# Kernel optimization log

Measured on AMD Instinct MI355X. Metric: run time of the kernel, lower is better.

Reference implementation:

```python
import jax, jax.numpy as jnp
import numpy as np

BITS = 4            # bits per quantized weight
NPACK = 8           # 32-bit container / 4-bit values
CBITS = 32          # compression dtype bit width (int32)
GROUP = 128         # quantization group size along in_features
IN = 4096
OUT = 11008
BATCH = 32


def _dequant(packed_weight, scale):
    # Unpack signed int4 values: (p << (32 - 4*(e+1))) >> 28, arithmetic shift
    # sign-extends, matching the torch recover() path for weight_dtype=int8.
    e = jnp.arange(NPACK, dtype=jnp.int32)                      # [8]
    shifted = (packed_weight[:, :, None] << (CBITS - BITS * (e + 1))) >> (CBITS - BITS)  # [O, I/8, 8]
    w_int = shifted.reshape(OUT, IN).astype(jnp.int8)           # signed int4 in int8
    # Per-group scale: reshape to [O*I/GROUP, GROUP] * [O*I/GROUP, 1]
    w = w_int.astype(jnp.float32).reshape(-1, GROUP) * scale.reshape(-1, 1)
    return w.reshape(OUT, IN)


def setup_inputs() -> dict:
    key = jax.random.key(0)
    k1, k2, k3, k4 = jax.random.split(key, 4)
    x = jax.random.normal(k1, (BATCH, IN), dtype=jnp.float32)
    packed_weight = jax.random.randint(
        k2, (OUT, IN // NPACK), jnp.iinfo(jnp.int32).min, jnp.iinfo(jnp.int32).max,
        dtype=jnp.int32)
    scale = jax.random.uniform(k3, (OUT, IN // GROUP), dtype=jnp.float32,
                               minval=0.001, maxval=0.02)
    bias = jax.random.normal(k4, (OUT,), dtype=jnp.float32)
    return {"x": x, "packed_weight": packed_weight, "scale": scale, "bias": bias}


def reference(x, packed_weight, scale, bias):
    W = _dequant(packed_weight, scale)      # [OUT, IN] fp32
    return x @ W.T + bias                    # F.linear(x, W, bias)
```

## Files before the change

kernel.cpp:

```cpp
#include <hip/hip_runtime.h>

#define IN_F   4096
#define OUT_F  11008
#define BATCH  32
#define NG     32
#define PACKS  512
#define SLICES 4
#define SLICE_F (BATCH * OUT_F)

typedef __bf16 bf16x8_t __attribute__((ext_vector_type(8)));
typedef float  floatx4_t __attribute__((ext_vector_type(4)));

__global__ __launch_bounds__(256) void prep_x(const float* __restrict__ x,
                                              unsigned short* __restrict__ xp) {
  int c  = blockIdx.x * 256 + threadIdx.x;
  int mm = c & 31;
  int k0 = ((c >> 5) & 3) * 32 + ((c >> 7) & 3) * 8 + (c >> 9) * 128;
  const float* src = x + mm * IN_F + k0;
  float4 f0 = *(const float4*)(src);
  float4 f1 = *(const float4*)(src + 4);
  float v[8] = {f0.x, f0.y, f0.z, f0.w, f1.x, f1.y, f1.z, f1.w};
  union { unsigned short s[8]; uint4 u; } r;
#pragma unroll
  for (int j = 0; j < 8; ++j) {
    unsigned int u = __float_as_uint(v[j]);
    unsigned int rnd = ((u >> 16) & 1u) + 0x7fffu;
    r.s[j] = (unsigned short)((u + rnd) >> 16);
  }
  *(uint4*)(xp + c * 8) = r.u;
}

__device__ inline bf16x8_t unpack8(int p) {
  union { unsigned short u[8]; bf16x8_t v; } r;
#pragma unroll
  for (int j = 0; j < 8; ++j) {
    int nib = (p << (28 - 4 * j)) >> 28;
    float f = (float)nib;
    r.u[j] = (unsigned short)(__float_as_uint(f) >> 16);
  }
  return r.v;
}

__device__ inline bf16x8_t load_frag(const unsigned short* p) {
  union { uint4 u; bf16x8_t v; } x;
  x.u = *(const uint4*)p;
  return x.v;
}

__global__ __launch_bounds__(512) void wql_part(
    const int* __restrict__ pw, const float* __restrict__ scale,
    const unsigned short* __restrict__ xp, float* __restrict__ part) {
  __shared__ float lds[8][BATCH * 32];

  const int tid = threadIdx.x;
  const int l   = tid & 63;
  const int w   = tid >> 6;
  const int col = l & 15;
  const int q   = l >> 4;
  const int n0  = blockIdx.x * 32;
  const int kc  = blockIdx.y;
  const int nA  = n0 + col;
  const int nB  = n0 + 16 + col;
  const int gg  = kc * 8 + w;

  int4 pA = *(const int4*)(pw + nA * PACKS + gg * 16 + q * 4);
  int4 pB = *(const int4*)(pw + nB * PACKS + gg * 16 + q * 4);
  float sA = scale[nA * NG + gg];
  float sB = scale[nB * NG + gg];

  const unsigned short* ab = xp + (gg * 512 + q * 32 + col) * 8;
  bf16x8_t a0[4], a1[4];
#pragma unroll
  for (int t = 0; t < 4; ++t) {
    a0[t] = load_frag(ab + t * 1024);
    a1[t] = load_frag(ab + t * 1024 + 128);
  }

  floatx4_t t00 = {0.f, 0.f, 0.f, 0.f};
  floatx4_t t01 = {0.f, 0.f, 0.f, 0.f};
  floatx4_t t10 = {0.f, 0.f, 0.f, 0.f};
  floatx4_t t11 = {0.f, 0.f, 0.f, 0.f};
  int pAv[4] = {pA.x, pA.y, pA.z, pA.w};
  int pBv[4] = {pB.x, pB.y, pB.z, pB.w};
#pragma unroll
  for (int t = 0; t < 4; ++t) {
    bf16x8_t b0 = unpack8(pAv[t]);
    bf16x8_t b1 = unpack8(pBv[t]);
    t00 = __builtin_amdgcn_mfma_f32_16x16x32_bf16(a0[t], b0, t00, 0, 0, 0);
    t10 = __builtin_amdgcn_mfma_f32_16x16x32_bf16(a1[t], b0, t10, 0, 0, 0);
    t01 = __builtin_amdgcn_mfma_f32_16x16x32_bf16(a0[t], b1, t01, 0, 0, 0);
    t11 = __builtin_amdgcn_mfma_f32_16x16x32_bf16(a1[t], b1, t11, 0, 0, 0);
  }

#pragma unroll
  for (int r = 0; r < 4; ++r) {
    int row = q * 4 + r;
    lds[w][row * 32 + col]             = t00[r] * sA;
    lds[w][row * 32 + 16 + col]        = t01[r] * sB;
    lds[w][(16 + row) * 32 + col]      = t10[r] * sA;
    lds[w][(16 + row) * 32 + 16 + col] = t11[r] * sB;
  }
  __syncthreads();

  float* wsp = part + kc * SLICE_F + n0;
  for (int e = tid; e < BATCH * 32; e += 512) {
    int row = e >> 5, cl = e & 31;
    float s = lds[0][e] + lds[1][e] + lds[2][e] + lds[3][e]
            + lds[4][e] + lds[5][e] + lds[6][e] + lds[7][e];
    wsp[row * OUT_F + cl] = s;
  }
}

__global__ __launch_bounds__(256) void reduce_out(
    const float* __restrict__ part, const float* __restrict__ bias,
    float* __restrict__ out) {
  int e4 = blockIdx.x * 256 + threadIdx.x;
  int e  = e4 << 2;
  int o  = e % OUT_F;
  float4 s = *(const float4*)(bias + o);
#pragma unroll
  for (int k = 0; k < SLICES; ++k) {
    float4 p = *(const float4*)(part + k * SLICE_F + e);
    s.x += p.x; s.y += p.y; s.z += p.z; s.w += p.w;
  }
  *(float4*)(out + e) = s;
}

extern "C" void kernel_launch(void* const* d_in, const int* in_sizes, int n_in,
                              void* d_out, int out_size, void* d_ws, size_t ws_size,
                              hipStream_t stream) {
  const float* x     = (const float*)d_in[0];
  const int*   pw    = (const int*)d_in[1];
  const float* scale = (const float*)d_in[2];
  const float* bias  = (const float*)d_in[3];
  float* out = (float*)d_out;
  unsigned short* xp = (unsigned short*)d_ws;
  float* part = (float*)((char*)d_ws + (1 << 20));

  hipLaunchKernelGGL(prep_x, dim3(16384 / 256), dim3(256), 0, stream, x, xp);
  hipLaunchKernelGGL(wql_part, dim3(OUT_F / 32, 4), dim3(512), 0, stream,
                     pw, scale, xp, part);
  hipLaunchKernelGGL(reduce_out, dim3(BATCH * OUT_F / 4 / 256), dim3(256), 0,
                     stream, part, bias, out);
}
```

Measured before the change: 85.11 us.

## Fuse x bf16 conversion into main kernel via swizzled LDS staging

Removes the separate prep_x launch. Each block now loads its 32x1024 slice of fp32 x, converts it to bf16 and writes it into a 64KB LDS buffer with an XOR swizzle to avoid bank conflicts. MFMA A fragments are then read from LDS, and the same buffer is reused for the partial-sum reduction. This saves one kernel launch and a global round trip, but every block now redoes the x conversion (344 column blocks per k-slice), and the 64KB of LDS per block lowers occupancy.

```diff
diff --git a/kernel.cpp b/kernel.cpp
--- a/kernel.cpp
+++ b/kernel.cpp
@@ -11,25 +11,6 @@
 typedef __bf16 bf16x8_t __attribute__((ext_vector_type(8)));
 typedef float  floatx4_t __attribute__((ext_vector_type(4)));
 
-__global__ __launch_bounds__(256) void prep_x(const float* __restrict__ x,
-                                              unsigned short* __restrict__ xp) {
-  int c  = blockIdx.x * 256 + threadIdx.x;
-  int mm = c & 31;
-  int k0 = ((c >> 5) & 3) * 32 + ((c >> 7) & 3) * 8 + (c >> 9) * 128;
-  const float* src = x + mm * IN_F + k0;
-  float4 f0 = *(const float4*)(src);
-  float4 f1 = *(const float4*)(src + 4);
-  float v[8] = {f0.x, f0.y, f0.z, f0.w, f1.x, f1.y, f1.z, f1.w};
-  union { unsigned short s[8]; uint4 u; } r;
-#pragma unroll
-  for (int j = 0; j < 8; ++j) {
-    unsigned int u = __float_as_uint(v[j]);
-    unsigned int rnd = ((u >> 16) & 1u) + 0x7fffu;
-    r.s[j] = (unsigned short)((u + rnd) >> 16);
-  }
-  *(uint4*)(xp + c * 8) = r.u;
-}
-
 __device__ inline bf16x8_t unpack8(int p) {
   union { unsigned short u[8]; bf16x8_t v; } r;
 #pragma unroll
@@ -41,16 +22,12 @@
   return r.v;
 }
 
-__device__ inline bf16x8_t load_frag(const unsigned short* p) {
-  union { uint4 u; bf16x8_t v; } x;
-  x.u = *(const uint4*)p;
-  return x.v;
-}
-
-__global__ __launch_bounds__(512) void wql_part(
+__global__ __launch_bounds__(512) void wql_main(
     const int* __restrict__ pw, const float* __restrict__ scale,
-    const unsigned short* __restrict__ xp, float* __restrict__ part) {
-  __shared__ float lds[8][BATCH * 32];
+    const float* __restrict__ x, float* __restrict__ part) {
+  __shared__ __align__(16) unsigned char lds_raw[65536];
+  unsigned short* xs = (unsigned short*)lds_raw;
+  float* park = (float*)lds_raw;
 
   const int tid = threadIdx.x;
   const int l   = tid & 63;
@@ -68,13 +45,33 @@
   float sA = scale[nA * NG + gg];
   float sB = scale[nB * NG + gg];
 
-  const unsigned short* ab = xp + (gg * 512 + q * 32 + col) * 8;
+  {
+    const int r = tid >> 4, s = tid & 15;
+    const float* xrow = x + r * IN_F + kc * 1024 + s * 8;
+#pragma unroll
+    for (int m = 0; m < 8; ++m) {
+      float4 f0 = *(const float4*)(xrow + m * 128);
+      float4 f1 = *(const float4*)(xrow + m * 128 + 4);
+      bf16x8_t v;
+      v[0] = (__bf16)f0.x; v[1] = (__bf16)f0.y;
+      v[2] = (__bf16)f0.z; v[3] = (__bf16)f0.w;
+      v[4] = (__bf16)f1.x; v[5] = (__bf16)f1.y;
+      v[6] = (__bf16)f1.z; v[7] = (__bf16)f1.w;
+      int u = (s + m * 16) ^ (r & 7);
+      *(bf16x8_t*)(xs + (r * 128 + u) * 8) = v;
+    }
+  }
+  __syncthreads();
+
   bf16x8_t a0[4], a1[4];
+  const int sw = col & 7;
 #pragma unroll
   for (int t = 0; t < 4; ++t) {
-    a0[t] = load_frag(ab + t * 1024);
-    a1[t] = load_frag(ab + t * 1024 + 128);
+    int u = (w * 16 + q * 4 + t) ^ sw;
+    a0[t] = *(const bf16x8_t*)(xs + (col * 128 + u) * 8);
+    a1[t] = *(const bf16x8_t*)(xs + ((col + 16) * 128 + u) * 8);
   }
+  __syncthreads();
 
   floatx4_t t00 = {0.f, 0.f, 0.f, 0.f};
   floatx4_t t01 = {0.f, 0.f, 0.f, 0.f};
@@ -92,21 +89,24 @@
     t11 = __builtin_amdgcn_mfma_f32_16x16x32_bf16(a1[t], b1, t11, 0, 0, 0);
   }
 
+  float* pk = park + w * 1024;
 #pragma unroll
   for (int r = 0; r < 4; ++r) {
     int row = q * 4 + r;
-    lds[w][row * 32 + col]             = t00[r] * sA;
-    lds[w][row * 32 + 16 + col]        = t01[r] * sB;
-    lds[w][(16 + row) * 32 + col]      = t10[r] * sA;
-    lds[w][(16 + row) * 32 + 16 + col] = t11[r] * sB;
+    pk[row * 32 + col]             = t00[r] * sA;
+    pk[row * 32 + 16 + col]        = t01[r] * sB;
+    pk[(16 + row) * 32 + col]      = t10[r] * sA;
+    pk[(16 + row) * 32 + 16 + col] = t11[r] * sB;
   }
   __syncthreads();
 
   float* wsp = part + kc * SLICE_F + n0;
   for (int e = tid; e < BATCH * 32; e += 512) {
     int row = e >> 5, cl = e & 31;
-    float s = lds[0][e] + lds[1][e] + lds[2][e] + lds[3][e]
-            + lds[4][e] + lds[5][e] + lds[6][e] + lds[7][e];
+    float s = park[0 * 1024 + e] + park[1 * 1024 + e]
+            + park[2 * 1024 + e] + park[3 * 1024 + e]
+            + park[4 * 1024 + e] + park[5 * 1024 + e]
+            + park[6 * 1024 + e] + park[7 * 1024 + e];
     wsp[row * OUT_F + cl] = s;
   }
 }
@@ -134,12 +134,10 @@
   const float* scale = (const float*)d_in[2];
   const float* bias  = (const float*)d_in[3];
   float* out = (float*)d_out;
-  unsigned short* xp = (unsigned short*)d_ws;
-  float* part = (float*)((char*)d_ws + (1 << 20));
+  float* part = (float*)d_ws;
 
-  hipLaunchKernelGGL(prep_x, dim3(16384 / 256), dim3(256), 0, stream, x, xp);
-  hipLaunchKernelGGL(wql_part, dim3(OUT_F / 32, 4), dim3(512), 0, stream,
-                     pw, scale, xp, part);
+  hipLaunchKernelGGL(wql_main, dim3(OUT_F / 32, 4), dim3(512), 0, stream,
+                     pw, scale, x, part);
   hipLaunchKernelGGL(reduce_out, dim3(BATCH * OUT_F / 4 / 256), dim3(256), 0,
                      stream, part, bias, out);
 }
```

Result: slower. 89.13 us (+4.7%).
